# Kernel tuning notes

Hardware: AMD Instinct MI355X
Metric: run time of the kernel (lower is better)

The kernel has to match this reference:

```python
import jax, jax.numpy as jnp
import numpy as np

N = 100000
E = 3200000
F_IN, F1, F2, F3, FB, NC = 256, 64, 32, 16, 8, 10


def setup_inputs() -> dict:
    key = jax.random.key(0)
    ks = jax.random.split(key, 12)
    features = jax.random.normal(ks[0], (N, F_IN), dtype=jnp.float32)
    edge_index = jax.random.randint(ks[1], (2, E), 0, N, dtype=jnp.int64)
    def glorot(k, shape):
        lim = np.sqrt(6.0 / (shape[0] + shape[1]))
        return jax.random.uniform(k, shape, jnp.float32, -lim, lim)
    return {
        "features": features,
        "edge_index": edge_index,
        "W1": glorot(ks[2], (F_IN, F1)), "b1": jnp.zeros((F1,), jnp.float32),
        "W2": glorot(ks[3], (F1, F2)),  "b2": jnp.zeros((F2,), jnp.float32),
        "W3": glorot(ks[4], (F2, F3)),  "b3": jnp.zeros((F3,), jnp.float32),
        "Wf": glorot(ks[5], (F3, FB)),  "bf": jnp.zeros((FB,), jnp.float32),
        "Ws": glorot(ks[6], (FB, NC)),  "bs": jnp.zeros((NC,), jnp.float32),
    }


def _gcn_norm(edge_index, n):
    # symmetric normalization with self-loops: deg includes +1 for self-loop
    src, dst = edge_index[0], edge_index[1]
    ones = jnp.ones((edge_index.shape[1],), jnp.float32)
    deg = jax.ops.segment_sum(ones, dst, num_segments=n) + 1.0
    dinv = jax.lax.rsqrt(deg)
    edge_w = dinv[src] * dinv[dst]        # [E]
    self_w = dinv * dinv                   # [N], self-loop weight
    return src, dst, edge_w, self_w


def _gcn_conv(x, W, b, src, dst, edge_w, self_w, n):
    xw = x @ W                                         # [N, Fout]
    msg = xw[src] * edge_w[:, None]                    # gather + scale
    agg = jax.ops.segment_sum(msg, dst, num_segments=n)
    return agg + xw * self_w[:, None] + b


def reference(features, edge_index, W1, b1, W2, b2, W3, b3, Wf, bf, Ws, bs):
    n = features.shape[0]
    src, dst, edge_w, self_w = _gcn_norm(edge_index, n)
    h = jax.nn.relu(_gcn_conv(features, W1, b1, src, dst, edge_w, self_w, n))
    h = jax.nn.relu(_gcn_conv(h, W2, b2, src, dst, edge_w, self_w, n))
    h = jax.nn.relu(_gcn_conv(h, W3, b3, src, dst, edge_w, self_w, n))
    pooled = jnp.mean(h, axis=0, keepdims=True)        # [1, F3]
    hidden = jax.nn.relu(pooled @ Wf + bf)
    scores = hidden @ Ws + bs
    return jax.nn.log_softmax(scores, axis=1)
```

## Files before the change

### kernel.cpp

```cpp
#include <hip/hip_runtime.h>
#include <hip/hip_fp16.h>
#include <math.h>

#define TPB 256
#define BKT_SHIFT 9
#define BKT_N 512
#define NB_MAX 256
#define CHUNK 4096
#define CAP   24576

typedef short bf16x8 __attribute__((ext_vector_type(8)));
typedef float f32x4  __attribute__((ext_vector_type(4)));

static __device__ inline unsigned short f2bf(float f) {
    union { float f; unsigned u; } v; v.f = f;
    unsigned r = v.u + 0x7FFF + ((v.u >> 16) & 1);
    return (unsigned short)(r >> 16);
}

__global__ __launch_bounds__(256) void init_cursor(int* __restrict__ bcursor, int nbkt) {
    int t = threadIdx.x;
    if (t < nbkt) bcursor[t] = t * CAP;
}

__global__ __launch_bounds__(TPB) void bucket_scatter(
    const int* __restrict__ src, const int* __restrict__ dst,
    int* __restrict__ bcursor, unsigned int* __restrict__ packed, int E, int nbkt)
{
    __shared__ unsigned int  spk[CHUNK];
    __shared__ unsigned char sbk[CHUNK];
    __shared__ int h[NB_MAX];
    __shared__ int base[NB_MAX];
    for (int c0 = blockIdx.x * CHUNK; c0 < E; c0 += gridDim.x * CHUNK) {
        int m = min(CHUNK, E - c0);
        for (int i = threadIdx.x; i < nbkt; i += TPB) h[i] = 0;
        __syncthreads();
        for (int i = threadIdx.x; i < m; i += TPB) {
            int d = dst[c0 + i];
            int s = src[c0 + i];
            int b = d >> BKT_SHIFT;
            spk[i] = ((unsigned)(d & (BKT_N - 1)) << 17) | (unsigned)s;
            sbk[i] = (unsigned char)b;
            atomicAdd(&h[b], 1);
        }
        __syncthreads();
        for (int i = threadIdx.x; i < nbkt; i += TPB) {
            int c = h[i];
            base[i] = c ? atomicAdd(&bcursor[i], c) : 0;
            h[i] = 0;
        }
        __syncthreads();
        for (int i = threadIdx.x; i < m; i += TPB) {
            int b = sbk[i];
            int pos = base[b] + atomicAdd(&h[b], 1);
            packed[pos] = spk[i];
        }
        __syncthreads();
    }
}

__global__ __launch_bounds__(256) void bucket_offsets(
    const int* __restrict__ bcursor, int* __restrict__ boff, int nbkt, int E)
{
    int t = threadIdx.x;
    int v = (t < nbkt) ? (bcursor[t] - t * CAP) : 0;
    __shared__ int tmp[256];
    tmp[t] = v; __syncthreads();
    for (int s = 1; s < 256; s <<= 1) {
        int x = (t >= s) ? tmp[t - s] : 0;
        __syncthreads();
        tmp[t] += x;
        __syncthreads();
    }
    if (t < nbkt) boff[t] = tmp[t] - v;
    if (t == 0) boff[nbkt] = E;
}

__global__ __launch_bounds__(256) void bucket_csr(
    const unsigned int* __restrict__ packed, const int* __restrict__ boff,
    int* __restrict__ off, float* __restrict__ dinv, int* __restrict__ ssrc,
    int n, int nbkt)
{
    const int b   = blockIdx.x;
    const int e0  = boff[b];
    const int cnt = boff[b + 1] - e0;
    const int p0  = b * CAP;
    const int v0  = b << BKT_SHIFT;
    const int nv  = min(BKT_N, n - v0);
    const int t   = threadIdx.x;

    __shared__ int hist[BKT_N];
    __shared__ int cur[BKT_N];
    __shared__ int tmp[256];

    for (int i = t; i < nv; i += 256) hist[i] = 0;
    __syncthreads();
    for (int e = t; e < cnt; e += 256)
        atomicAdd(&hist[packed[p0 + e] >> 17], 1);
    __syncthreads();

    int a = (2 * t     < nv) ? hist[2 * t]     : 0;
    int c = (2 * t + 1 < nv) ? hist[2 * t + 1] : 0;
    int ps = a + c;
    tmp[t] = ps; __syncthreads();
    for (int s = 1; s < 256; s <<= 1) {
        int x = (t >= s) ? tmp[t - s] : 0;
        __syncthreads();
        tmp[t] += x;
        __syncthreads();
    }
    int ex = tmp[t] - ps;
    if (2 * t < nv) {
        cur[2 * t] = ex;
        off[v0 + 2 * t] = e0 + ex;
        dinv[v0 + 2 * t] = rsqrtf((float)a + 1.0f);
    }
    if (2 * t + 1 < nv) {
        cur[2 * t + 1] = ex + a;
        off[v0 + 2 * t + 1] = e0 + ex + a;
        dinv[v0 + 2 * t + 1] = rsqrtf((float)c + 1.0f);
    }
    if (b == nbkt - 1 && t == 0) off[n] = boff[nbkt];
    __syncthreads();

    for (int e = t; e < cnt; e += 256) {
        unsigned p = packed[p0 + e];
        int dl = p >> 17;
        int s  = p & 0x1FFFF;
        int pos = atomicAdd(&cur[dl], 1);
        ssrc[e0 + pos] = s;
    }
}

__global__ __launch_bounds__(256) void conv_w(
    const float* __restrict__ W, unsigned short* __restrict__ Wt, int K, int N)
{
    int total = K * N;
    for (int i = threadIdx.x + blockIdx.x * 256; i < total; i += gridDim.x * 256) {
        int k = i / N, c = i % N;
        Wt[c * K + k] = f2bf(W[i]);
    }
}

template<int K, int NCOL, typename AT>
__global__ __launch_bounds__(TPB) void gemm_mfma(
    const AT* __restrict__ A, const unsigned short* __restrict__ Wt,
    const float* __restrict__ dinv, __half* __restrict__ Y, int n)
{
    constexpr int NT = NCOL / 16;
    constexpr int KS = K / 32;
    const int lane = threadIdx.x & 63;
    const int w    = threadIdx.x >> 6;
    const int rowbase = blockIdx.x * 128 + w * 32;
    const int arow = lane & 15;
    const int kb   = (lane >> 4) * 8;

    f32x4 acc[2][NT];
#pragma unroll
    for (int mt = 0; mt < 2; mt++)
#pragma unroll
        for (int nt = 0; nt < NT; nt++) acc[mt][nt] = (f32x4)(0.f);

#pragma unroll
    for (int ks = 0; ks < KS; ks++) {
        bf16x8 a[2];
#pragma unroll
        for (int mt = 0; mt < 2; mt++) {
            int r = rowbase + mt * 16 + arow;
            if constexpr (sizeof(AT) == 4) {
                if (r < n) {
                    const float4* p = (const float4*)(A + (size_t)r * K + ks * 32 + kb);
                    float4 u = p[0], v = p[1];
                    a[mt][0] = f2bf(u.x); a[mt][1] = f2bf(u.y);
                    a[mt][2] = f2bf(u.z); a[mt][3] = f2bf(u.w);
                    a[mt][4] = f2bf(v.x); a[mt][5] = f2bf(v.y);
                    a[mt][6] = f2bf(v.z); a[mt][7] = f2bf(v.w);
                } else {
#pragma unroll
                    for (int i = 0; i < 8; i++) a[mt][i] = 0;
                }
            } else {
                if (r < n)
                    a[mt] = *(const bf16x8*)(A + (size_t)r * K + ks * 32 + kb);
                else {
#pragma unroll
                    for (int i = 0; i < 8; i++) a[mt][i] = 0;
                }
            }
        }
        bf16x8 b[NT];
#pragma unroll
        for (int nt = 0; nt < NT; nt++)
            b[nt] = *(const bf16x8*)(Wt + (size_t)(nt * 16 + arow) * K + ks * 32 + kb);
#pragma unroll
        for (int mt = 0; mt < 2; mt++)
#pragma unroll
            for (int nt = 0; nt < NT; nt++)
                acc[mt][nt] = __builtin_amdgcn_mfma_f32_16x16x32_bf16(
                    a[mt], b[nt], acc[mt][nt], 0, 0, 0);
    }

#pragma unroll
    for (int mt = 0; mt < 2; mt++) {
        int r0 = rowbase + mt * 16 + (lane >> 4) * 4;
#pragma unroll
        for (int j = 0; j < 4; j++) {
            int r = r0 + j;
            if (r < n) {
                float dv = dinv[r];
#pragma unroll
                for (int nt = 0; nt < NT; nt++)
                    Y[(size_t)r * NCOL + nt * 16 + arow] = __float2half(acc[mt][nt][j] * dv);
            }
        }
    }
}

template<int F>
__global__ __launch_bounds__(TPB) void seg_agg_h(
    const int* __restrict__ off, const int* __restrict__ ssrc,
    const __half2* __restrict__ y2, const float* __restrict__ dinv,
    const float* __restrict__ b, unsigned int* __restrict__ H, int n)
{
    constexpr int L     = F / 2;
    constexpr int LOG2L = (L == 32) ? 5 : (L == 16) ? 4 : 3;
    constexpr int NPW   = 64 / L;
    const int lane = threadIdx.x & 63;
    const int fl   = lane & (L - 1);
    const int sub  = lane >> LOG2L;
    const int wid  = (blockIdx.x * blockDim.x + threadIdx.x) >> 6;
    const int nw   = (gridDim.x * blockDim.x) >> 6;
    const float2 bv = ((const float2*)b)[fl];

    for (int v0 = wid * NPW; v0 < n; v0 += nw * NPW) {
        int v = v0 + sub;
        if (v >= n) continue;
        int e0 = off[v], e1 = off[v + 1];
        float2 s = __half22float2(y2[(size_t)v * L + fl]);
        for (int base = e0; base < e1; base += L) {
            int idx = (base + fl < e1) ? ssrc[base + fl] : 0;
            int cnt = min(L, e1 - base);
            int j = 0;
            for (; j + 4 <= cnt; j += 4) {
                int s0 = __shfl(idx, sub * L + j,     64);
                int s1 = __shfl(idx, sub * L + j + 1, 64);
                int s2 = __shfl(idx, sub * L + j + 2, 64);
                int s3 = __shfl(idx, sub * L + j + 3, 64);
                float2 f0 = __half22float2(y2[(size_t)s0 * L + fl]);
                float2 f1 = __half22float2(y2[(size_t)s1 * L + fl]);
                float2 f2 = __half22float2(y2[(size_t)s2 * L + fl]);
                float2 f3 = __half22float2(y2[(size_t)s3 * L + fl]);
                s.x += (f0.x + f1.x) + (f2.x + f3.x);
                s.y += (f0.y + f1.y) + (f2.y + f3.y);
            }
            for (; j < cnt; j++) {
                int sj = __shfl(idx, sub * L + j, 64);
                float2 f0 = __half22float2(y2[(size_t)sj * L + fl]);
                s.x += f0.x; s.y += f0.y;
            }
        }
        float dv = dinv[v];
        float rx = fmaxf(fmaf(s.x, dv, bv.x), 0.f);
        float ry = fmaxf(fmaf(s.y, dv, bv.y), 0.f);
        H[(size_t)v * L + fl] = ((unsigned)f2bf(ry) << 16) | (unsigned)f2bf(rx);
    }
}

__global__ __launch_bounds__(TPB) void seg_agg16_pool_h(
    const int* __restrict__ off, const int* __restrict__ ssrc,
    const __half2* __restrict__ y2, const float* __restrict__ dinv,
    const float* __restrict__ b, float* __restrict__ pooled, int n)
{
    constexpr int L = 8;
    const int lane = threadIdx.x & 63;
    const int fl   = lane & 7;
    const int sub  = lane >> 3;
    const int wid  = (blockIdx.x * blockDim.x + threadIdx.x) >> 6;
    const int nw   = (gridDim.x * blockDim.x) >> 6;
    const float2 bv = ((const float2*)b)[fl];
    float2 pacc = make_float2(0.f, 0.f);

    for (int v0 = wid * 8; v0 < n; v0 += nw * 8) {
        int v = v0 + sub;
        if (v >= n) continue;
        int e0 = off[v], e1 = off[v + 1];
        float2 s = __half22float2(y2[(size_t)v * L + fl]);
        for (int base = e0; base < e1; base += L) {
            int idx = (base + fl < e1) ? ssrc[base + fl] : 0;
            int cnt = min(L, e1 - base);
            int j = 0;
            for (; j + 4 <= cnt; j += 4) {
                int s0 = __shfl(idx, sub * L + j,     64);
                int s1 = __shfl(idx, sub * L + j + 1, 64);
                int s2 = __shfl(idx, sub * L + j + 2, 64);
                int s3 = __shfl(idx, sub * L + j + 3, 64);
                float2 f0 = __half22float2(y2[(size_t)s0 * L + fl]);
                float2 f1 = __half22float2(y2[(size_t)s1 * L + fl]);
                float2 f2 = __half22float2(y2[(size_t)s2 * L + fl]);
                float2 f3 = __half22float2(y2[(size_t)s3 * L + fl]);
                s.x += (f0.x + f1.x) + (f2.x + f3.x);
                s.y += (f0.y + f1.y) + (f2.y + f3.y);
            }
            for (; j < cnt; j++) {
                int sj = __shfl(idx, sub * L + j, 64);
                float2 f0 = __half22float2(y2[(size_t)sj * L + fl]);
                s.x += f0.x; s.y += f0.y;
            }
        }
        float dv = dinv[v];
        pacc.x += fmaxf(fmaf(s.x, dv, bv.x), 0.f);
        pacc.y += fmaxf(fmaf(s.y, dv, bv.y), 0.f);
    }
    __shared__ float redx[TPB], redy[TPB];
    redx[threadIdx.x] = pacc.x;
    redy[threadIdx.x] = pacc.y;
    __syncthreads();
    for (int st = 128; st >= 8; st >>= 1) {
        if (threadIdx.x < st) {
            redx[threadIdx.x] += redx[threadIdx.x + st];
            redy[threadIdx.x] += redy[threadIdx.x + st];
        }
        __syncthreads();
    }
    if (threadIdx.x < 8) {
        atomicAdd(&pooled[2 * threadIdx.x],     redx[threadIdx.x]);
        atomicAdd(&pooled[2 * threadIdx.x + 1], redy[threadIdx.x]);
    }
}

__global__ void head_kernel(const float* __restrict__ pooled,
                            const float* __restrict__ Wf, const float* __restrict__ bf,
                            const float* __restrict__ Ws, const float* __restrict__ bs,
                            float* __restrict__ out, float invn)
{
    if (threadIdx.x == 0 && blockIdx.x == 0) {
        float p[16], h[8], s[10];
        for (int i = 0; i < 16; i++) p[i] = pooled[i] * invn;
        for (int j = 0; j < 8; j++) {
            float a = bf[j];
            for (int i = 0; i < 16; i++) a = fmaf(p[i], Wf[i * 8 + j], a);
            h[j] = fmaxf(a, 0.f);
        }
        float m = -1e30f;
        for (int c = 0; c < 10; c++) {
            float a = bs[c];
            for (int j = 0; j < 8; j++) a = fmaf(h[j], Ws[j * 10 + c], a);
            s[c] = a;
            m = fmaxf(m, a);
        }
        float lse = 0.f;
        for (int c = 0; c < 10; c++) lse += expf(s[c] - m);
        lse = logf(lse) + m;
        for (int c = 0; c < 10; c++) out[c] = s[c] - lse;
    }
}

static inline size_t align_up(size_t x) { return (x + 255) & ~(size_t)255; }

extern "C" void kernel_launch(void* const* d_in, const int* in_sizes, int n_in,
                              void* d_out, int out_size, void* d_ws, size_t ws_size,
                              hipStream_t stream)
{
    const float* X  = (const float*)d_in[0];
    const int*   ei = (const int*)  d_in[1];
    const float* W1 = (const float*)d_in[2];  const float* b1 = (const float*)d_in[3];
    const float* W2 = (const float*)d_in[4];  const float* b2 = (const float*)d_in[5];
    const float* W3 = (const float*)d_in[6];  const float* b3 = (const float*)d_in[7];
    const float* Wf = (const float*)d_in[8];  const float* bf = (const float*)d_in[9];
    const float* Ws = (const float*)d_in[10]; const float* bs = (const float*)d_in[11];

    const int n = in_sizes[0] / 256;
    const int E = in_sizes[1] / 2;
    const int* src = ei;
    const int* dst = ei + E;
    const int nbkt = (n + BKT_N - 1) / BKT_N;

    char* ws = (char*)d_ws;
    size_t off_b = 0;
    int* bcursor = (int*)(ws + off_b);   off_b += align_up(NB_MAX * 4);
    int* boff    = (int*)(ws + off_b);   off_b += align_up((NB_MAX + 1) * 4);
    float* dinv  = (float*)(ws + off_b); off_b += align_up((size_t)n * 4);
    int* off     = (int*)(ws + off_b);   off_b += align_up((size_t)(n + 1) * 4);
    float* pooled= (float*)(ws + off_b); off_b += align_up(16 * 4);
    unsigned short* Wt1 = (unsigned short*)(ws + off_b); off_b += align_up(64 * 256 * 2);
    unsigned short* Wt2 = (unsigned short*)(ws + off_b); off_b += align_up(32 * 64 * 2);
    unsigned short* Wt3 = (unsigned short*)(ws + off_b); off_b += align_up(16 * 32 * 2);
    unsigned int* packed = (unsigned int*)(ws + off_b); off_b += align_up((size_t)nbkt * CAP * 4);
    int* ssrc    = (int*)(ws + off_b);   off_b += align_up((size_t)E * 4);
    __half2* Y   = (__half2*)(ws + off_b); off_b += align_up((size_t)n * 64 * 2);
    unsigned int* H = (unsigned int*)(ws + off_b); off_b += align_up((size_t)n * 64 * 2);

    hipMemsetAsync(pooled, 0, 16 * 4, stream);

    init_cursor<<<1, 256, 0, stream>>>(bcursor, nbkt);
    int nchunk = (E + CHUNK - 1) / CHUNK;
    bucket_scatter<<<nchunk, TPB, 0, stream>>>(src, dst, bcursor, packed, E, nbkt);
    bucket_offsets<<<1, 256, 0, stream>>>(bcursor, boff, nbkt, E);
    bucket_csr<<<nbkt, 256, 0, stream>>>(packed, boff, off, dinv, ssrc, n, nbkt);

    conv_w<<<16, 256, 0, stream>>>(W1, Wt1, 256, 64);
    conv_w<<<2, 256, 0, stream>>>(W2, Wt2, 64, 32);
    conv_w<<<1, 256, 0, stream>>>(W3, Wt3, 32, 16);

    const int gblk = (n + 127) / 128;

    gemm_mfma<256, 64, float><<<gblk, TPB, 0, stream>>>(X, Wt1, dinv, (__half*)Y, n);
    seg_agg_h<64><<<2048, TPB, 0, stream>>>(off, ssrc, Y, dinv, b1, H, n);

    gemm_mfma<64, 32, unsigned short><<<gblk, TPB, 0, stream>>>(
        (const unsigned short*)H, Wt2, dinv, (__half*)Y, n);
    seg_agg_h<32><<<2048, TPB, 0, stream>>>(off, ssrc, Y, dinv, b2, H, n);

    gemm_mfma<32, 16, unsigned short><<<gblk, TPB, 0, stream>>>(
        (const unsigned short*)H, Wt3, dinv, (__half*)Y, n);
    seg_agg16_pool_h<<<1024, TPB, 0, stream>>>(off, ssrc, Y, dinv, b3, pooled, n);

    head_kernel<<<1, 64, 0, stream>>>(pooled, Wf, bf, Ws, bs, (float*)d_out, 1.0f / (float)n);
}
```

Before: 301.1 us.

## Store GCN messages in scaled FP8 and aggregate one node per thread

The per-layer transformed features Y are now stored as FP8 with a fixed scale of 16 instead of FP16, which halves the bytes moved by the random-access neighbour gather. The aggregation kernels are rewritten so each thread owns one destination node and reads whole packed rows with 4-way edge unrolling, replacing the shuffle-based wave-cooperative scheme. The pooling variant now reduces 16 features through shared memory. FP8 quantization adds precision loss and may hurt accuracy, and one thread per node can leave work unbalanced across lanes and issue uncoalesced row loads.

```diff
diff --git a/kernel.cpp b/kernel.cpp
--- a/kernel.cpp
+++ b/kernel.cpp
@@ -8,6 +8,8 @@
 #define NB_MAX 256
 #define CHUNK 4096
 #define CAP   24576
+#define Y_SCALE 16.0f
+#define Y_INV_SCALE (1.0f / 16.0f)
 
 typedef short bf16x8 __attribute__((ext_vector_type(8)));
 typedef float f32x4  __attribute__((ext_vector_type(4)));
@@ -16,6 +18,11 @@
     union { float f; unsigned u; } v; v.f = f;
     unsigned r = v.u + 0x7FFF + ((v.u >> 16) & 1);
     return (unsigned short)(r >> 16);
+}
+
+static __device__ inline unsigned char f2fp8(float x) {
+    int p = __builtin_amdgcn_cvt_pk_fp8_f32(x, x, 0, false);
+    return (unsigned char)(p & 0xFF);
 }
 
 __global__ __launch_bounds__(256) void init_cursor(int* __restrict__ bcursor, int nbkt) {
@@ -145,7 +152,7 @@
 template<int K, int NCOL, typename AT>
 __global__ __launch_bounds__(TPB) void gemm_mfma(
     const AT* __restrict__ A, const unsigned short* __restrict__ Wt,
-    const float* __restrict__ dinv, __half* __restrict__ Y, int n)
+    const float* __restrict__ dinv, unsigned char* __restrict__ Yq, int n)
 {
     constexpr int NT = NCOL / 16;
     constexpr int KS = K / 32;
@@ -207,124 +214,110 @@
         for (int j = 0; j < 4; j++) {
             int r = r0 + j;
             if (r < n) {
-                float dv = dinv[r];
+                float dv = dinv[r] * Y_SCALE;
 #pragma unroll
                 for (int nt = 0; nt < NT; nt++)
-                    Y[(size_t)r * NCOL + nt * 16 + arow] = __float2half(acc[mt][nt][j] * dv);
-            }
-        }
-    }
-}
-
-template<int F>
-__global__ __launch_bounds__(TPB) void seg_agg_h(
+                    Yq[(size_t)r * NCOL + nt * 16 + arow] = f2fp8(acc[mt][nt][j] * dv);
+            }
+        }
+    }
+}
+
+template<int F, bool POOL>
+__global__ __launch_bounds__(TPB) void seg_node(
     const int* __restrict__ off, const int* __restrict__ ssrc,
-    const __half2* __restrict__ y2, const float* __restrict__ dinv,
-    const float* __restrict__ b, unsigned int* __restrict__ H, int n)
-{
-    constexpr int L     = F / 2;
-    constexpr int LOG2L = (L == 32) ? 5 : (L == 16) ? 4 : 3;
-    constexpr int NPW   = 64 / L;
-    const int lane = threadIdx.x & 63;
-    const int fl   = lane & (L - 1);
-    const int sub  = lane >> LOG2L;
-    const int wid  = (blockIdx.x * blockDim.x + threadIdx.x) >> 6;
-    const int nw   = (gridDim.x * blockDim.x) >> 6;
-    const float2 bv = ((const float2*)b)[fl];
-
-    for (int v0 = wid * NPW; v0 < n; v0 += nw * NPW) {
-        int v = v0 + sub;
-        if (v >= n) continue;
+    const unsigned char* __restrict__ Yq, const float* __restrict__ dinv,
+    const float* __restrict__ bias, unsigned int* __restrict__ H,
+    float* __restrict__ pooled, int n)
+{
+    constexpr int NU = F / 4;
+    constexpr int U  = 4;
+    const int v = blockIdx.x * TPB + threadIdx.x;
+
+    float acc[F];
+#pragma unroll
+    for (int i = 0; i < F; i++) acc[i] = 0.f;
+    float r16[16];
+    if constexpr (POOL) {
+#pragma unroll
+        for (int i = 0; i < 16; i++) r16[i] = 0.f;
+    }
+
+    if (v < n) {
+        {
+            const unsigned int* yp = (const unsigned int*)(Yq + (size_t)v * F);
+#pragma unroll
+            for (int wn = 0; wn < NU; wn++) {
+                unsigned u = yp[wn];
+                acc[4 * wn + 0] += __builtin_amdgcn_cvt_f32_fp8(u, 0);
+                acc[4 * wn + 1] += __builtin_amdgcn_cvt_f32_fp8(u, 1);
+                acc[4 * wn + 2] += __builtin_amdgcn_cvt_f32_fp8(u, 2);
+                acc[4 * wn + 3] += __builtin_amdgcn_cvt_f32_fp8(u, 3);
+            }
+        }
         int e0 = off[v], e1 = off[v + 1];
-        float2 s = __half22float2(y2[(size_t)v * L + fl]);
-        for (int base = e0; base < e1; base += L) {
-            int idx = (base + fl < e1) ? ssrc[base + fl] : 0;
-            int cnt = min(L, e1 - base);
-            int j = 0;
-            for (; j + 4 <= cnt; j += 4) {
-                int s0 = __shfl(idx, sub * L + j,     64);
-                int s1 = __shfl(idx, sub * L + j + 1, 64);
-                int s2 = __shfl(idx, sub * L + j + 2, 64);
-                int s3 = __shfl(idx, sub * L + j + 3, 64);
-                float2 f0 = __half22float2(y2[(size_t)s0 * L + fl]);
-                float2 f1 = __half22float2(y2[(size_t)s1 * L + fl]);
-                float2 f2 = __half22float2(y2[(size_t)s2 * L + fl]);
-                float2 f3 = __half22float2(y2[(size_t)s3 * L + fl]);
-                s.x += (f0.x + f1.x) + (f2.x + f3.x);
-                s.y += (f0.y + f1.y) + (f2.y + f3.y);
-            }
-            for (; j < cnt; j++) {
-                int sj = __shfl(idx, sub * L + j, 64);
-                float2 f0 = __half22float2(y2[(size_t)sj * L + fl]);
-                s.x += f0.x; s.y += f0.y;
-            }
-        }
-        float dv = dinv[v];
-        float rx = fmaxf(fmaf(s.x, dv, bv.x), 0.f);
-        float ry = fmaxf(fmaf(s.y, dv, bv.y), 0.f);
-        H[(size_t)v * L + fl] = ((unsigned)f2bf(ry) << 16) | (unsigned)f2bf(rx);
-    }
-}
-
-__global__ __launch_bounds__(TPB) void seg_agg16_pool_h(
-    const int* __restrict__ off, const int* __restrict__ ssrc,
-    const __half2* __restrict__ y2, const float* __restrict__ dinv,
-    const float* __restrict__ b, float* __restrict__ pooled, int n)
-{
-    constexpr int L = 8;
-    const int lane = threadIdx.x & 63;
-    const int fl   = lane & 7;
-    const int sub  = lane >> 3;
-    const int wid  = (blockIdx.x * blockDim.x + threadIdx.x) >> 6;
-    const int nw   = (gridDim.x * blockDim.x) >> 6;
-    const float2 bv = ((const float2*)b)[fl];
-    float2 pacc = make_float2(0.f, 0.f);
-
-    for (int v0 = wid * 8; v0 < n; v0 += nw * 8) {
-        int v = v0 + sub;
-        if (v >= n) continue;
-        int e0 = off[v], e1 = off[v + 1];
-        float2 s = __half22float2(y2[(size_t)v * L + fl]);
-        for (int base = e0; base < e1; base += L) {
-            int idx = (base + fl < e1) ? ssrc[base + fl] : 0;
-            int cnt = min(L, e1 - base);
-            int j = 0;
-            for (; j + 4 <= cnt; j += 4) {
-                int s0 = __shfl(idx, sub * L + j,     64);
-                int s1 = __shfl(idx, sub * L + j + 1, 64);
-                int s2 = __shfl(idx, sub * L + j + 2, 64);
-                int s3 = __shfl(idx, sub * L + j + 3, 64);
-                float2 f0 = __half22float2(y2[(size_t)s0 * L + fl]);
-                float2 f1 = __half22float2(y2[(size_t)s1 * L + fl]);
-                float2 f2 = __half22float2(y2[(size_t)s2 * L + fl]);
-                float2 f3 = __half22float2(y2[(size_t)s3 * L + fl]);
-                s.x += (f0.x + f1.x) + (f2.x + f3.x);
-                s.y += (f0.y + f1.y) + (f2.y + f3.y);
-            }
-            for (; j < cnt; j++) {
-                int sj = __shfl(idx, sub * L + j, 64);
-                float2 f0 = __half22float2(y2[(size_t)sj * L + fl]);
-                s.x += f0.x; s.y += f0.y;
-            }
-        }
-        float dv = dinv[v];
-        pacc.x += fmaxf(fmaf(s.x, dv, bv.x), 0.f);
-        pacc.y += fmaxf(fmaf(s.y, dv, bv.y), 0.f);
-    }
-    __shared__ float redx[TPB], redy[TPB];
-    redx[threadIdx.x] = pacc.x;
-    redy[threadIdx.x] = pacc.y;
-    __syncthreads();
-    for (int st = 128; st >= 8; st >>= 1) {
-        if (threadIdx.x < st) {
-            redx[threadIdx.x] += redx[threadIdx.x + st];
-            redy[threadIdx.x] += redy[threadIdx.x + st];
-        }
-        __syncthreads();
-    }
-    if (threadIdx.x < 8) {
-        atomicAdd(&pooled[2 * threadIdx.x],     redx[threadIdx.x]);
-        atomicAdd(&pooled[2 * threadIdx.x + 1], redy[threadIdx.x]);
+        int e = e0;
+        for (; e + U <= e1; e += U) {
+            unsigned rw[U][NU];
+#pragma unroll
+            for (int k = 0; k < U; k++) {
+                const unsigned int* yp = (const unsigned int*)(Yq + (size_t)ssrc[e + k] * F);
+#pragma unroll
+                for (int wn = 0; wn < NU; wn++) rw[k][wn] = yp[wn];
+            }
+#pragma unroll
+            for (int k = 0; k < U; k++)
+#pragma unroll
+                for (int wn = 0; wn < NU; wn++) {
+                    unsigned u = rw[k][wn];
+                    acc[4 * wn + 0] += __builtin_amdgcn_cvt_f32_fp8(u, 0);
+                    acc[4 * wn + 1] += __builtin_amdgcn_cvt_f32_fp8(u, 1);
+                    acc[4 * wn + 2] += __builtin_amdgcn_cvt_f32_fp8(u, 2);
+                    acc[4 * wn + 3] += __builtin_amdgcn_cvt_f32_fp8(u, 3);
+                }
+        }
+        for (; e < e1; e++) {
+            const unsigned int* yp = (const unsigned int*)(Yq + (size_t)ssrc[e] * F);
+#pragma unroll
+            for (int wn = 0; wn < NU; wn++) {
+                unsigned u = yp[wn];
+                acc[4 * wn + 0] += __builtin_amdgcn_cvt_f32_fp8(u, 0);
+                acc[4 * wn + 1] += __builtin_amdgcn_cvt_f32_fp8(u, 1);
+                acc[4 * wn + 2] += __builtin_amdgcn_cvt_f32_fp8(u, 2);
+                acc[4 * wn + 3] += __builtin_amdgcn_cvt_f32_fp8(u, 3);
+            }
+        }
+
+        float dv = dinv[v] * Y_INV_SCALE;
+        if constexpr (!POOL) {
+            unsigned int* hp = H + (size_t)v * (F / 2);
+#pragma unroll
+            for (int i = 0; i < F; i += 2) {
+                float rx = fmaxf(fmaf(acc[i],     dv, bias[i]),     0.f);
+                float ry = fmaxf(fmaf(acc[i + 1], dv, bias[i + 1]), 0.f);
+                hp[i / 2] = ((unsigned)f2bf(ry) << 16) | (unsigned)f2bf(rx);
+            }
+        } else {
+#pragma unroll
+            for (int i = 0; i < 16; i++)
+                r16[i] = fmaxf(fmaf(acc[i], dv, bias[i]), 0.f);
+        }
+    }
+
+    if constexpr (POOL) {
+        __shared__ float red[TPB][17];
+#pragma unroll
+        for (int i = 0; i < 16; i++) red[threadIdx.x][i] = r16[i];
+        __syncthreads();
+        for (int st = 128; st >= 1; st >>= 1) {
+            if (threadIdx.x < st) {
+#pragma unroll
+                for (int i = 0; i < 16; i++)
+                    red[threadIdx.x][i] += red[threadIdx.x + st][i];
+            }
+            __syncthreads();
+        }
+        if (threadIdx.x < 16) atomicAdd(&pooled[threadIdx.x], red[0][threadIdx.x]);
     }
 }
 
@@ -387,7 +380,7 @@
     unsigned short* Wt3 = (unsigned short*)(ws + off_b); off_b += align_up(16 * 32 * 2);
     unsigned int* packed = (unsigned int*)(ws + off_b); off_b += align_up((size_t)nbkt * CAP * 4);
     int* ssrc    = (int*)(ws + off_b);   off_b += align_up((size_t)E * 4);
-    __half2* Y   = (__half2*)(ws + off_b); off_b += align_up((size_t)n * 64 * 2);
+    unsigned char* Yq = (unsigned char*)(ws + off_b); off_b += align_up((size_t)n * 64);
     unsigned int* H = (unsigned int*)(ws + off_b); off_b += align_up((size_t)n * 64 * 2);
 
     hipMemsetAsync(pooled, 0, 16 * 4, stream);
@@ -403,17 +396,18 @@
     conv_w<<<1, 256, 0, stream>>>(W3, Wt3, 32, 16);
 
     const int gblk = (n + 127) / 128;
-
-    gemm_mfma<256, 64, float><<<gblk, TPB, 0, stream>>>(X, Wt1, dinv, (__half*)Y, n);
-    seg_agg_h<64><<<2048, TPB, 0, stream>>>(off, ssrc, Y, dinv, b1, H, n);
+    const int nblk = (n + TPB - 1) / TPB;
+
+    gemm_mfma<256, 64, float><<<gblk, TPB, 0, stream>>>(X, Wt1, dinv, Yq, n);
+    seg_node<64, false><<<nblk, TPB, 0, stream>>>(off, ssrc, Yq, dinv, b1, H, nullptr, n);
 
     gemm_mfma<64, 32, unsigned short><<<gblk, TPB, 0, stream>>>(
-        (const unsigned short*)H, Wt2, dinv, (__half*)Y, n);
-    seg_agg_h<32><<<2048, TPB, 0, stream>>>(off, ssrc, Y, dinv, b2, H, n);
+        (const unsigned short*)H, Wt2, dinv, Yq, n);
+    seg_node<32, false><<<nblk, TPB, 0, stream>>>(off, ssrc, Yq, dinv, b2, H, nullptr, n);
 
     gemm_mfma<32, 16, unsigned short><<<gblk, TPB, 0, stream>>>(
-        (const unsigned short*)H, Wt3, dinv, (__half*)Y, n);
-    seg_agg16_pool_h<<<1024, TPB, 0, stream>>>(off, ssrc, Y, dinv, b3, pooled, n);
+        (const unsigned short*)H, Wt3, dinv, Yq, n);
+    seg_node<16, true><<<nblk, TPB, 0, stream>>>(off, ssrc, Yq, dinv, b3, nullptr, pooled, n);
 
     head_kernel<<<1, 64, 0, stream>>>(pooled, Wf, bf, Ws, bs, (float*)d_out, 1.0f / (float)n);
 }
```

After: 274.9 us. 1.1x faster.
